# Kernel tuning notes

Hardware: AMD Instinct MI355X
Metric: run time of the kernel (lower is better)

Reference implementation:

```python
import jax, jax.numpy as jnp
import numpy as np
from jax import lax

DIM = 192
HEADS = 4
HIDDEN = int(DIM * 2.66)  # 510
B, H, W = 2, 64, 64
EPS_LN = 1e-6
EPS_NORM = 1e-12


def conv1x1(x, w, b):
    # x: (b,c,h,w), w: (o,c), b: (o,)
    return jnp.einsum('bchw,oc->bohw', x, w) + b[None, :, None, None]


def dwconv3x3(x, w, b):
    # depthwise 3x3, SAME padding; w: (C,1,3,3)
    c = x.shape[1]
    y = lax.conv_general_dilated(x, w, window_strides=(1, 1), padding='SAME',
                                 feature_group_count=c,
                                 dimension_numbers=('NCHW', 'OIHW', 'NCHW'))
    return y + b[None, :, None, None]


def layernorm2d(x, w, b):
    mean = jnp.mean(x, axis=(2, 3), keepdims=True)
    var = jnp.mean((x - mean) ** 2, axis=(2, 3), keepdims=True)
    return (x - mean) / jnp.sqrt(var + EPS_LN) * w[None, :, None, None] + b[None, :, None, None]


def mdta(x, qkv_w, qkv_b, qkv_dw_w, qkv_dw_b, temperature, proj_w, proj_b):
    b, c, h, w = x.shape
    qkv = dwconv3x3(conv1x1(x, qkv_w, qkv_b), qkv_dw_w, qkv_dw_b)
    q, k, v = jnp.split(qkv, 3, axis=1)
    dh = c // HEADS
    q = q.reshape(b, HEADS, dh, h * w)
    k = k.reshape(b, HEADS, dh, h * w)
    v = v.reshape(b, HEADS, dh, h * w)
    # L2-normalize over per-head channel dim (axis=2), like F.normalize(dim=2)
    q = q / jnp.maximum(jnp.linalg.norm(q, axis=2, keepdims=True), EPS_NORM)
    k = k / jnp.maximum(jnp.linalg.norm(k, axis=2, keepdims=True), EPS_NORM)
    # spatial attention map: (b, heads, HW, HW)
    attn = jnp.einsum('bhcn,bhcm->bhnm', q, k) * temperature[None]  # temp (heads,1,1)
    attn = jax.nn.softmax(attn, axis=-1)
    out = jnp.einsum('bhnm,bhcm->bhcn', attn, v)  # (b,heads,dh,HW)
    out = out.reshape(b, c, h, w)
    return conv1x1(out, proj_w, proj_b)


def gdfn(x, pin_w, pin_b, dw_w, dw_b, pout_w, pout_b):
    y = dwconv3x3(conv1x1(x, pin_w, pin_b), dw_w, dw_b)
    y1, y2 = jnp.split(y, 2, axis=1)
    y = jax.nn.gelu(y1, approximate=False) * y2
    return conv1x1(y, pout_w, pout_b)


def setup_inputs() -> dict:
    key = jax.random.key(0)
    ks = jax.random.split(key, 8)
    s = 0.02
    return {
        'x': jax.random.normal(ks[0], (B, DIM, H, W), jnp.float32),
        'ln1_w': jnp.ones((DIM,), jnp.float32),
        'ln1_b': jnp.zeros((DIM,), jnp.float32),
        'qkv_w': jax.random.normal(ks[1], (DIM * 3, DIM), jnp.float32) * s,
        'qkv_b': jnp.zeros((DIM * 3,), jnp.float32),
        'qkv_dw_w': jax.random.normal(ks[2], (DIM * 3, 1, 3, 3), jnp.float32) * s,
        'qkv_dw_b': jnp.zeros((DIM * 3,), jnp.float32),
        'temperature': jnp.ones((HEADS, 1, 1), jnp.float32),
        'proj_w': jax.random.normal(ks[3], (DIM, DIM), jnp.float32) * s,
        'proj_b': jnp.zeros((DIM,), jnp.float32),
        'ln2_w': jnp.ones((DIM,), jnp.float32),
        'ln2_b': jnp.zeros((DIM,), jnp.float32),
        'pin_w': jax.random.normal(ks[4], (HIDDEN * 2, DIM), jnp.float32) * s,
        'pin_b': jnp.zeros((HIDDEN * 2,), jnp.float32),
        'gdfn_dw_w': jax.random.normal(ks[5], (HIDDEN * 2, 1, 3, 3), jnp.float32) * s,
        'gdfn_dw_b': jnp.zeros((HIDDEN * 2,), jnp.float32),
        'pout_w': jax.random.normal(ks[6], (DIM, HIDDEN), jnp.float32) * s,
        'pout_b': jnp.zeros((DIM,), jnp.float32),
    }


def reference(x, ln1_w, ln1_b, qkv_w, qkv_b, qkv_dw_w, qkv_dw_b, temperature,
              proj_w, proj_b, ln2_w, ln2_b, pin_w, pin_b, gdfn_dw_w, gdfn_dw_b,
              pout_w, pout_b):
    x = x + mdta(layernorm2d(x, ln1_w, ln1_b), qkv_w, qkv_b, qkv_dw_w, qkv_dw_b,
                 temperature, proj_w, proj_b)
    x = x + gdfn(layernorm2d(x, ln2_w, ln2_b), pin_w, pin_b, gdfn_dw_w, gdfn_dw_b,
                 pout_w, pout_b)
    return x
```

## Files before the change

### kernel.cpp

```cpp
#include <hip/hip_runtime.h>
#include <hip/hip_bf16.h>

typedef __bf16 bf16x8 __attribute__((ext_vector_type(8)));
typedef __bf16 bf16x4 __attribute__((ext_vector_type(4)));
typedef __bf16 bf16x2 __attribute__((ext_vector_type(2)));
typedef float f32x4 __attribute__((ext_vector_type(4)));

#define HW 4096
#define DIMC 192
#define DH 48
#define HIDC 510
#define LOG2E 1.44269504088896f

__device__ __forceinline__ float exp2_fast(float x) {
#if __has_builtin(__builtin_amdgcn_exp2f)
  return __builtin_amdgcn_exp2f(x);
#else
  float r;
  asm("v_exp_f32 %0, %1\n\ts_nop 1" : "=v"(r) : "v"(x));
  return r;
#endif
}

__device__ __forceinline__ float rcp_fast(float x) {
#if __has_builtin(__builtin_amdgcn_rcpf)
  return __builtin_amdgcn_rcpf(x);
#else
  float r;
  asm("v_rcp_f32 %0, %1\n\ts_nop 1" : "=v"(r) : "v"(x));
  return r;
#endif
}

__device__ __forceinline__ float gelu_fast(float x) {
  float z = fabsf(x) * 0.70710678118654752f;
  float t = rcp_fast(fmaf(0.3275911f, z, 1.f));
  float p = t * fmaf(t, fmaf(t, fmaf(t, fmaf(t, 1.061405429f, -1.453152027f), 1.421413741f), -0.284496736f), 0.254829592f);
  float e = exp2_fast(-z * z * 1.4426950408889634f);
  float erfa = 1.f - p * e;
  float erfx = copysignf(erfa, x);
  return 0.5f * x * (1.f + erfx);
}

__global__ __launch_bounds__(256) void wcvt_ln_kernel(const float* __restrict__ qkv_w, const float* __restrict__ proj_w,
                                                      const float* __restrict__ pin_w, const float* __restrict__ pout_w,
                                                      __bf16* __restrict__ wb_qkv, __bf16* __restrict__ wb_proj,
                                                      __bf16* __restrict__ wb_pin, __bf16* __restrict__ wb_pout,
                                                      const float* __restrict__ x, const float* __restrict__ lw,
                                                      const float* __restrict__ lb, float* __restrict__ sc,
                                                      float* __restrict__ sh) {
  __shared__ float red[8];
  if (blockIdx.x < 1725) {
    int idx = blockIdx.x * 256 + threadIdx.x;
    if (idx < 110592) {
      wb_qkv[idx] = (__bf16)qkv_w[idx];
    } else if (idx < 147456) {
      int i = idx - 110592;
      wb_proj[i] = (__bf16)proj_w[i];
    } else if (idx < 343296) {
      int i = idx - 147456;
      wb_pin[i] = (__bf16)pin_w[i];
    } else if (idx < 441600) {
      int i = idx - 343296;
      int o = i >> 9, c = i & 511;
      wb_pout[i] = (c < HIDC) ? (__bf16)pout_w[o * HIDC + c] : (__bf16)0.f;
    }
    return;
  }
  int bc = blockIdx.x - 1725;
  int c = bc % DIMC;
  const float* row = x + (size_t)bc * HW;
  float s = 0.f, s2 = 0.f;
  for (int i = threadIdx.x * 4; i < HW; i += 1024) {
    f32x4 v = *(const f32x4*)&row[i];
    s += (v.x + v.y) + (v.z + v.w);
    s2 = fmaf(v.x, v.x, s2); s2 = fmaf(v.y, v.y, s2);
    s2 = fmaf(v.z, v.z, s2); s2 = fmaf(v.w, v.w, s2);
  }
  for (int off = 32; off; off >>= 1) { s += __shfl_down(s, off, 64); s2 += __shfl_down(s2, off, 64); }
  int wid = threadIdx.x >> 6;
  if ((threadIdx.x & 63) == 0) { red[wid] = s; red[4 + wid] = s2; }
  __syncthreads();
  if (threadIdx.x == 0) {
    s = red[0] + red[1] + red[2] + red[3];
    s2 = red[4] + red[5] + red[6] + red[7];
    float mean = s * (1.f / HW);
    float var = s2 * (1.f / HW) - mean * mean;
    float rstd = rsqrtf(var + 1e-6f);
    float scv = rstd * lw[c];
    sc[bc] = scv;
    sh[bc] = lb[c] - mean * scv;
  }
}

__global__ __launch_bounds__(256) void ln_stats_kernel(const float* __restrict__ x, const float* __restrict__ w,
                                                       const float* __restrict__ b, float* __restrict__ sc,
                                                       float* __restrict__ sh) {
  int bc = blockIdx.x;
  int c = bc % DIMC;
  const float* row = x + (size_t)bc * HW;
  float s = 0.f, s2 = 0.f;
  for (int i = threadIdx.x * 4; i < HW; i += 1024) {
    f32x4 v = *(const f32x4*)&row[i];
    s += (v.x + v.y) + (v.z + v.w);
    s2 = fmaf(v.x, v.x, s2); s2 = fmaf(v.y, v.y, s2);
    s2 = fmaf(v.z, v.z, s2); s2 = fmaf(v.w, v.w, s2);
  }
  __shared__ float red[8];
  for (int off = 32; off; off >>= 1) { s += __shfl_down(s, off, 64); s2 += __shfl_down(s2, off, 64); }
  int wid = threadIdx.x >> 6;
  if ((threadIdx.x & 63) == 0) { red[wid] = s; red[4 + wid] = s2; }
  __syncthreads();
  if (threadIdx.x == 0) {
    s = red[0] + red[1] + red[2] + red[3];
    s2 = red[4] + red[5] + red[6] + red[7];
    float mean = s * (1.f / HW);
    float var = s2 * (1.f / HW) - mean * mean;
    float rstd = rsqrtf(var + 1e-6f);
    float scv = rstd * w[c];
    sc[bc] = scv;
    sh[bc] = b[c] - mean * scv;
  }
}

__global__ __launch_bounds__(256) void ln_apply_t_kernel(const float* __restrict__ x, const float* __restrict__ sc,
                                                         const float* __restrict__ sh, __bf16* __restrict__ Xt) {
  int n0 = blockIdx.x * 64, c0 = blockIdx.y * 32, b = blockIdx.z;
  int t = threadIdx.x;
  int n = t & 63, cs = c0 + (t >> 6) * 8;
  __bf16 ob[8];
#pragma unroll
  for (int cc = 0; cc < 8; ++cc) {
    int c = cs + cc;
    float v = fmaf(x[((size_t)(b * DIMC + c)) * HW + n0 + n], sc[b * DIMC + c], sh[b * DIMC + c]);
    ob[cc] = (__bf16)v;
  }
  *(bf16x8*)&Xt[((size_t)((b << 12) + n0 + n)) * DIMC + cs] = *(bf16x8*)ob;
}

__global__ __launch_bounds__(256) void gemm_kernel(const __bf16* __restrict__ A, const __bf16* __restrict__ Bt,
                                                   const float* __restrict__ bias, const float* __restrict__ res,
                                                   float* __restrict__ outf, __bf16* __restrict__ outb,
                                                   const float* __restrict__ part,
                                                   int O, int Cs, int mode) {
  __shared__ __align__(16) __bf16 Asub[64 * 72];
  __shared__ __align__(16) __bf16 Bsub[128 * 72];
  __shared__ float linvS[4][128];
  const int t = threadIdx.x;
  const int lane = t & 63, wv = t >> 6;
  const int q4 = lane >> 4, l16 = lane & 15;
  int o0 = blockIdx.y * 64;
  if (o0 + 64 > O) o0 = O - 64;
  const int ntot0 = blockIdx.x * 128;
  const int b = ntot0 >> 12;
  const int n_in_b0 = ntot0 & 4095;

  if (mode == 4) {
#pragma unroll
    for (int jj = 0; jj < 2; ++jj) {
      int id = t + 256 * jj;
      int h = id >> 7, nl = id & 127;
      int n_in_b = n_in_b0 + nl;
      int ntb = n_in_b >> 6, n64 = n_in_b & 63;
      size_t pb = ((size_t)((b * 4 + h) * 64 + ntb)) * 3136 + 3072 + n64;
      float s = part[pb] + part[pb + (size_t)512 * 3136];
      linvS[h][nl] = rcp_fast(s);
    }
  }

  f32x4 acc[8];
#pragma unroll
  for (int nt = 0; nt < 8; ++nt) acc[nt] = (f32x4){0.f, 0.f, 0.f, 0.f};

  for (int c0 = 0; c0 < Cs; c0 += 64) {
    __syncthreads();
#pragma unroll
    for (int j = 0; j < 2; ++j) {
      int id = t + 256 * j;
      *(bf16x8*)&Asub[(id >> 3) * 72 + (id & 7) * 8] =
          *(const bf16x8*)&A[((size_t)(o0 + (id >> 3))) * Cs + c0 + (id & 7) * 8];
    }
    if (mode == 4) {
#pragma unroll
      for (int j = 0; j < 4; ++j) {
        int id = t + 256 * j;
        int row = id >> 3, cgrp = id & 7;
        int cglob = c0 + cgrp * 8;
        int h = cglob / 48;
        int cc = cglob - h * 48;
        int n_in_b = n_in_b0 + row;
        int ntb = n_in_b >> 6, n64 = n_in_b & 63;
        size_t pb = ((size_t)((b * 4 + h) * 64 + ntb)) * 3136 + (size_t)n64 * 48 + cc;
        f32x4 a0 = *(const f32x4*)&part[pb];
        f32x4 a1 = *(const f32x4*)&part[pb + 4];
        f32x4 b0 = *(const f32x4*)&part[pb + (size_t)512 * 3136];
        f32x4 b1 = *(const f32x4*)&part[pb + (size_t)512 * 3136 + 4];
        float li = linvS[h][row];
        f32x4 s0 = (a0 + b0) * li;
        f32x4 s1 = (a1 + b1) * li;
        bf16x8 ov = { (__bf16)s0.x, (__bf16)s0.y, (__bf16)s0.z, (__bf16)s0.w,
                      (__bf16)s1.x, (__bf16)s1.y, (__bf16)s1.z, (__bf16)s1.w };
        *(bf16x8*)&Bsub[row * 72 + cgrp * 8] = ov;
      }
    } else if (mode != 3) {
#pragma unroll
      for (int j = 0; j < 4; ++j) {
        int id = t + 256 * j;
        *(bf16x8*)&Bsub[(id >> 3) * 72 + (id & 7) * 8] =
            *(const bf16x8*)&Bt[((size_t)(ntot0 + (id >> 3))) * Cs + c0 + (id & 7) * 8];
      }
    } else {
      int cr = t & 63, seg = t >> 6;
      int cg = c0 + cr;
      __bf16 tmp[32];
      if (cg < HIDC) {
        const __bf16* gp = Bt + ((size_t)(b * HIDC + cg)) * HW + n_in_b0 + seg * 32;
#pragma unroll
        for (int j = 0; j < 4; ++j) *(bf16x8*)&tmp[8 * j] = *(const bf16x8*)&gp[8 * j];
      } else {
#pragma unroll
        for (int k = 0; k < 32; ++k) tmp[k] = (__bf16)0.f;
      }
#pragma unroll
      for (int k = 0; k < 32; ++k) Bsub[(seg * 32 + k) * 72 + cr] = tmp[k];
    }
    __syncthreads();
#pragma unroll
    for (int ks = 0; ks < 2; ++ks) {
      bf16x8 af = *(const bf16x8*)&Asub[(16 * wv + l16) * 72 + 32 * ks + 8 * q4];
#pragma unroll
      for (int nt = 0; nt < 8; ++nt) {
        bf16x8 bfr = *(const bf16x8*)&Bsub[(16 * nt + l16) * 72 + 32 * ks + 8 * q4];
        acc[nt] = __builtin_amdgcn_mfma_f32_16x16x32_bf16(af, bfr, acc[nt], 0, 0, 0);
      }
    }
  }

  float bvals[4];
#pragma unroll
  for (int r = 0; r < 4; ++r) bvals[r] = bias[o0 + 16 * wv + 4 * q4 + r];
#pragma unroll
  for (int nt = 0; nt < 8; ++nt) {
    int n_in_b = n_in_b0 + 16 * nt + l16;
#pragma unroll
    for (int r = 0; r < 4; ++r) {
      int o = o0 + 16 * wv + 4 * q4 + r;
      size_t addr = ((size_t)(b * O + o)) * HW + n_in_b;
      float v = acc[nt][r] + bvals[r];
      if (mode >= 2) { outf[addr] = v + res[addr]; }
      else if (mode == 0) { outf[addr] = v; }
      else { outb[addr] = (__bf16)v; }
    }
  }
}

__global__ __launch_bounds__(256) void dwconv_split_kernel(const __bf16* __restrict__ in, const float* __restrict__ w,
                                                           const float* __restrict__ bias,
                                                           __bf16* __restrict__ qdwb, __bf16* __restrict__ Vbf) {
  int bc = blockIdx.x;
  int b = bc / 576, ch = bc - b * 576;
  __shared__ float tile[66 * 68];
  for (int i = threadIdx.x; i < 66 * 68; i += 256) tile[i] = 0.f;
  __syncthreads();
  const __bf16* p = in + (size_t)bc * HW;
  for (int j = 0; j < 8; ++j) {
    int i = 2 * threadIdx.x + 512 * j;
    bf16x2 v = *(const bf16x2*)&p[i];
    int y = i >> 6, xx = i & 63;
    tile[(y + 1) * 68 + xx + 1] = (float)v.x;
    tile[(y + 1) * 68 + xx + 2] = (float)v.y;
  }
  __syncthreads();
  float w0 = w[ch * 9 + 0], w1 = w[ch * 9 + 1], w2 = w[ch * 9 + 2];
  float w3 = w[ch * 9 + 3], w4 = w[ch * 9 + 4], w5 = w[ch * 9 + 5];
  float w6 = w[ch * 9 + 6], w7 = w[ch * 9 + 7], w8 = w[ch * 9 + 8];
  float bb = bias[ch];
  __bf16* dst;
  if (ch < 384) dst = qdwb + ((size_t)(b * 384 + ch)) * HW;
  else {
    int c = ch - 384, h = c / DH, cc = c - h * DH;
    dst = Vbf + ((size_t)((b * 4 + h) * DH + cc)) * HW;
  }
  for (int j = 0; j < 8; ++j) {
    int i = 2 * threadIdx.x + 512 * j;
    int y = i >> 6, xx = i & 63;
    const float* tt = &tile[y * 68 + xx];
    float a = bb;
    a = fmaf(w0, tt[0], a);   a = fmaf(w1, tt[1], a);   a = fmaf(w2, tt[2], a);
    a = fmaf(w3, tt[68], a);  a = fmaf(w4, tt[69], a);  a = fmaf(w5, tt[70], a);
    a = fmaf(w6, tt[136], a); a = fmaf(w7, tt[137], a); a = fmaf(w8, tt[138], a);
    float a2 = bb;
    a2 = fmaf(w0, tt[1], a2);   a2 = fmaf(w1, tt[2], a2);   a2 = fmaf(w2, tt[3], a2);
    a2 = fmaf(w3, tt[69], a2);  a2 = fmaf(w4, tt[70], a2);  a2 = fmaf(w5, tt[71], a2);
    a2 = fmaf(w6, tt[137], a2); a2 = fmaf(w7, tt[138], a2); a2 = fmaf(w8, tt[139], a2);
    bf16x2 o = { (__bf16)a, (__bf16)a2 };
    *(bf16x2*)&dst[i] = o;
  }
}

__global__ __launch_bounds__(256) void gdfn_dw_gate_kernel(const __bf16* __restrict__ hid, const float* __restrict__ w,
                                                           const float* __restrict__ bias, __bf16* __restrict__ gate) {
  int blk = blockIdx.x;
  int b = blk / HIDC, j = blk - b * HIDC;
  __shared__ __align__(16) float t1[66 * 68];
  __shared__ __align__(16) float t2[66 * 68];
  const int tid = threadIdx.x;
  if (tid < 136) {
    int r = (tid >= 68) ? 65 : 0;
    int c = (tid >= 68) ? tid - 68 : tid;
    t1[r * 68 + c] = 0.f;
    t2[r * 68 + c] = 0.f;
  }
  {
    int r = (tid >> 2) + 1;
    int c4 = tid & 3;
    int c = (c4 == 0) ? 0 : 64 + c4;
    t1[r * 68 + c] = 0.f;
    t2[r * 68 + c] = 0.f;
  }
  const __bf16* p1 = hid + ((size_t)b * (2 * HIDC) + j) * HW;
  const __bf16* p2 = p1 + (size_t)HIDC * HW;
  for (int jj = 0; jj < 8; ++jj) {
    int i = 2 * tid + 512 * jj;
    bf16x2 v1 = *(const bf16x2*)&p1[i];
    bf16x2 v2 = *(const bf16x2*)&p2[i];
    int y = i >> 6, xx = i & 63;
    t1[(y + 1) * 68 + xx + 1] = (float)v1.x;
    t1[(y + 1) * 68 + xx + 2] = (float)v1.y;
    t2[(y + 1) * 68 + xx + 1] = (float)v2.x;
    t2[(y + 1) * 68 + xx + 2] = (float)v2.y;
  }
  __syncthreads();
  int c1 = j, c2 = j + HIDC;
  float wa[9], wb[9];
#pragma unroll
  for (int k = 0; k < 9; ++k) { wa[k] = w[c1 * 9 + k]; wb[k] = w[c2 * 9 + k]; }
  float bi1 = bias[c1], bi2 = bias[c2];

  const int y = tid >> 2, x0 = 16 * (tid & 3);
  float x1v[16], x2v[16];
#pragma unroll
  for (int p = 0; p < 16; ++p) { x1v[p] = bi1; x2v[p] = bi2; }
#pragma unroll
  for (int r = 0; r < 3; ++r) {
    const float* rp1 = &t1[(y + r) * 68 + x0];
    float rr[20];
#pragma unroll
    for (int q = 0; q < 5; ++q) *(f32x4*)&rr[4 * q] = *(const f32x4*)&rp1[4 * q];
    float w0 = wa[3 * r], w1 = wa[3 * r + 1], w2 = wa[3 * r + 2];
#pragma unroll
    for (int p = 0; p < 16; ++p)
      x1v[p] = fmaf(w0, rr[p], fmaf(w1, rr[p + 1], fmaf(w2, rr[p + 2], x1v[p])));
  }
#pragma unroll
  for (int r = 0; r < 3; ++r) {
    const float* rp2 = &t2[(y + r) * 68 + x0];
    float rr[20];
#pragma unroll
    for (int q = 0; q < 5; ++q) *(f32x4*)&rr[4 * q] = *(const f32x4*)&rp2[4 * q];
    float w0 = wb[3 * r], w1 = wb[3 * r + 1], w2 = wb[3 * r + 2];
#pragma unroll
    for (int p = 0; p < 16; ++p)
      x2v[p] = fmaf(w0, rr[p], fmaf(w1, rr[p + 1], fmaf(w2, rr[p + 2], x2v[p])));
  }
  __bf16 ob[16];
#pragma unroll
  for (int p = 0; p < 16; ++p) ob[p] = (__bf16)(gelu_fast(x1v[p]) * x2v[p]);
  __bf16* op = gate + ((size_t)b * HIDC + j) * HW + y * 64 + x0;
  *(bf16x8*)&op[0] = *(bf16x8*)&ob[0];
  *(bf16x8*)&op[8] = *(bf16x8*)&ob[8];
}

__global__ __launch_bounds__(256) void prep_qk_kernel(const __bf16* __restrict__ qdwb, const float* __restrict__ temp,
                                                      __bf16* __restrict__ Qbf, __bf16* __restrict__ Kbf) {
  int t2 = blockIdx.x * 256 + threadIdx.x;
  int bh = t2 >> 11;
  int np = (t2 & 2047) * 2;
  int b = bh >> 2, h = bh & 3;
  const int isK = blockIdx.y;
  const __bf16* sp = qdwb + ((size_t)(b * 384 + isK * 192 + h * DH)) * HW + np;
  float tq = isK ? 1.f : temp[h] * LOG2E;

  bf16x2 raw[DH];
  float ss0 = 0.f, ss1 = 0.f;
#pragma unroll
  for (int c = 0; c < DH; ++c) {
    bf16x2 v = *(const bf16x2*)&sp[(size_t)c * HW];
    raw[c] = v;
    float f0 = (float)v.x, f1 = (float)v.y;
    ss0 = fmaf(f0, f0, ss0);
    ss1 = fmaf(f1, f1, ss1);
  }
  float sc0 = tq / fmaxf(sqrtf(ss0), 1e-12f);
  float sc1 = tq / fmaxf(sqrtf(ss1), 1e-12f);
  __bf16 ob0[64], ob1[64];
#pragma unroll
  for (int c = 0; c < DH; ++c) {
    ob0[c] = (__bf16)((float)raw[c].x * sc0);
    ob1[c] = (__bf16)((float)raw[c].y * sc1);
  }
#pragma unroll
  for (int c = DH; c < 64; ++c) { ob0[c] = (__bf16)0.f; ob1[c] = (__bf16)0.f; }
  __bf16* dd = (isK ? Kbf : Qbf) + ((size_t)(bh << 12) + np) * 64;
#pragma unroll
  for (int ch = 0; ch < 8; ++ch) {
    *(bf16x8*)&dd[ch * 8] = *(bf16x8*)&ob0[ch * 8];
    *(bf16x8*)&dd[64 + ch * 8] = *(bf16x8*)&ob1[ch * 8];
  }
}

__global__ __launch_bounds__(256) void attn_split_kernel(const __bf16* __restrict__ Qbf, const __bf16* __restrict__ Kbf,
                                                         const __bf16* __restrict__ Vbf, float* __restrict__ part) {
  __shared__ __align__(16) __bf16 Vc[2][48 * 72];
  __shared__ __align__(16) __bf16 Pl[2][64 * 72];
  const int tid = threadIdx.x;
  const int lane = tid & 63;
  const int wv = tid >> 6;
  const int q4 = lane >> 4, l16 = lane & 15;
  const int bid = blockIdx.x;
  const int chunk = bid >> 9, rest = bid & 511;
  const int bh = rest >> 6, nt = rest & 63;
  const int n0 = nt * 64;
  const __bf16* Qg = Qbf + (size_t)bh * HW * 64;
  const __bf16* Kg = Kbf + (size_t)bh * HW * 64;
  const __bf16* Vg = Vbf + (size_t)bh * DH * HW;

  bf16x8 qf[4][2];
#pragma unroll
  for (int s = 0; s < 4; ++s)
#pragma unroll
    for (int ks = 0; ks < 2; ++ks)
      qf[s][ks] = *(const bf16x8*)&Qg[((size_t)(n0 + 16 * s + l16)) * 64 + 32 * ks + 8 * q4];

  const int m0 = chunk * 2048;
  const __bf16* kp0 = Kg + ((size_t)(m0 + 16 * wv + l16)) * 64 + 8 * q4;
  const __bf16* kp1 = kp0 + 32;
  const __bf16* vp0 = Vg + ((size_t)(tid >> 3)) * HW + m0 + (tid & 7) * 8;
  const __bf16* vp1 = Vg + ((size_t)((tid + 256) >> 3)) * HW + m0 + ((tid + 256) & 7) * 8;
  bf16x8 kf0 = *(const bf16x8*)kp0;
  bf16x8 kf1 = *(const bf16x8*)kp1;
  bf16x8 vreg[2];
  vreg[0] = *(const bf16x8*)vp0;
  if (tid < 128) vreg[1] = *(const bf16x8*)vp1;

  float lsub[4] = {0.f, 0.f, 0.f, 0.f};
  f32x4 oacc[3];
#pragma unroll
  for (int ct = 0; ct < 3; ++ct) oacc[ct] = (f32x4){0.f, 0.f, 0.f, 0.f};

  for (int it = 0; it < 32; ++it) {
    const int cur = it & 1;
    *(bf16x8*)&Vc[cur][(tid >> 3) * 72 + (tid & 7) * 8] = vreg[0];
    if (tid < 128) {
      int i = tid + 256;
      *(bf16x8*)&Vc[cur][(i >> 3) * 72 + (i & 7) * 8] = vreg[1];
    }
    kp0 += 4096; kp1 += 4096; vp0 += 64; vp1 += 64;
    bf16x8 kn0 = *(const bf16x8*)kp0;
    bf16x8 kn1 = *(const bf16x8*)kp1;
    vreg[0] = *(const bf16x8*)vp0;
    if (tid < 128) vreg[1] = *(const bf16x8*)vp1;

    f32x4 sacc[4];
#pragma unroll
    for (int s = 0; s < 4; ++s) sacc[s] = (f32x4){0.f, 0.f, 0.f, 0.f};
    __builtin_amdgcn_s_setprio(1);
#pragma unroll
    for (int s = 0; s < 4; ++s)
      sacc[s] = __builtin_amdgcn_mfma_f32_16x16x32_bf16(kf0, qf[s][0], sacc[s], 0, 0, 0);
#pragma unroll
    for (int s = 0; s < 4; ++s)
      sacc[s] = __builtin_amdgcn_mfma_f32_16x16x32_bf16(kf1, qf[s][1], sacc[s], 0, 0, 0);
    __builtin_amdgcn_s_setprio(0);

#pragma unroll
    for (int s = 0; s < 4; ++s) {
      float p0 = exp2_fast(sacc[s][0]);
      float p1 = exp2_fast(sacc[s][1]);
      float p2 = exp2_fast(sacc[s][2]);
      float p3 = exp2_fast(sacc[s][3]);
      lsub[s] += (p0 + p1) + (p2 + p3);
      bf16x4 pk = { (__bf16)p0, (__bf16)p1, (__bf16)p2, (__bf16)p3 };
      *(bf16x4*)&Pl[cur][(16 * s + l16) * 72 + 16 * wv + 4 * q4] = pk;
    }
    __syncthreads();

    __builtin_amdgcn_s_setprio(1);
#pragma unroll
    for (int ks = 0; ks < 2; ++ks) {
      bf16x8 pf = *(const bf16x8*)&Pl[cur][(16 * wv + l16) * 72 + 32 * ks + 8 * q4];
#pragma unroll
      for (int ct = 0; ct < 3; ++ct) {
        bf16x8 vf = *(const bf16x8*)&Vc[cur][(16 * ct + l16) * 72 + 32 * ks + 8 * q4];
        oacc[ct] = __builtin_amdgcn_mfma_f32_16x16x32_bf16(pf, vf, oacc[ct], 0, 0, 0);
      }
    }
    __builtin_amdgcn_s_setprio(0);
    kf0 = kn0; kf1 = kn1;
  }

  __syncthreads();
  float* Lred = (float*)&Pl[0][0];
#pragma unroll
  for (int s = 0; s < 4; ++s) {
    float v = lsub[s];
    v += __shfl_xor(v, 16, 64);
    v += __shfl_xor(v, 32, 64);
    if (q4 == 0) Lred[wv * 64 + 16 * s + l16] = v;
  }
  __syncthreads();
  size_t pbase = (size_t)bid * 3136;
  if (tid < 64)
    part[pbase + 3072 + tid] = Lred[tid] + Lred[64 + tid] + Lred[128 + tid] + Lred[192 + tid];
#pragma unroll
  for (int ct = 0; ct < 3; ++ct)
#pragma unroll
    for (int r = 0; r < 4; ++r) {
      int n = 16 * wv + 4 * q4 + r;
      part[pbase + (size_t)n * 48 + 16 * ct + l16] = oacc[ct][r];
    }
}

extern "C" void kernel_launch(void* const* d_in, const int* in_sizes, int n_in,
                              void* d_out, int out_size, void* d_ws, size_t ws_size,
                              hipStream_t stream) {
  const float* x        = (const float*)d_in[0];
  const float* ln1_w    = (const float*)d_in[1];
  const float* ln1_b    = (const float*)d_in[2];
  const float* qkv_w    = (const float*)d_in[3];
  const float* qkv_b    = (const float*)d_in[4];
  const float* qkv_dw_w = (const float*)d_in[5];
  const float* qkv_dw_b = (const float*)d_in[6];
  const float* temperature = (const float*)d_in[7];
  const float* proj_w   = (const float*)d_in[8];
  const float* proj_b   = (const float*)d_in[9];
  const float* ln2_w    = (const float*)d_in[10];
  const float* ln2_b    = (const float*)d_in[11];
  const float* pin_w    = (const float*)d_in[12];
  const float* pin_b    = (const float*)d_in[13];
  const float* gdfn_dw_w = (const float*)d_in[14];
  const float* gdfn_dw_b = (const float*)d_in[15];
  const float* pout_w   = (const float*)d_in[16];
  const float* pout_b   = (const float*)d_in[17];
  float* out = (float*)d_out;
  float* ws = (float*)d_ws;

  __bf16* wb_qkv  = (__bf16*)(ws + 0);
  __bf16* wb_proj = (__bf16*)(ws + 55296);
  __bf16* wb_pin  = (__bf16*)(ws + 73728);
  __bf16* wb_pout = (__bf16*)(ws + 171648);
  float* sc1 = ws + 220800;
  float* sh1 = ws + 221184;
  float* sc2 = ws + 221568;
  float* sh2 = ws + 221952;
  __bf16* Xt1 = (__bf16*)(ws + 222336);
  __bf16* Xt2 = (__bf16*)(ws + 222336);
  __bf16* Qbf = (__bf16*)(ws + 222336);
  __bf16* Kbf = (__bf16*)(ws + 1270912);
  __bf16* Vbf = (__bf16*)(ws + 2319488);
  __bf16* qkvb   = (__bf16*)(ws + 3105920);
  __bf16* hid    = (__bf16*)(ws + 3105920);
  __bf16* qdwb  = (__bf16*)(ws + 5465216);
  float*  Opart = ws + 5465216;
  __bf16* gate  = (__bf16*)(ws + 7283840);

  wcvt_ln_kernel<<<1725 + 2 * DIMC, 256, 0, stream>>>(qkv_w, proj_w, pin_w, pout_w,
                                                      wb_qkv, wb_proj, wb_pin, wb_pout,
                                                      x, ln1_w, ln1_b, sc1, sh1);
  ln_apply_t_kernel<<<dim3(64, 6, 2), 256, 0, stream>>>(x, sc1, sh1, Xt1);
  gemm_kernel<<<dim3(64, 9), 256, 0, stream>>>(wb_qkv, Xt1, qkv_b, nullptr, nullptr, qkvb, nullptr, 576, 192, 1);
  dwconv_split_kernel<<<1152, 256, 0, stream>>>(qkvb, qkv_dw_w, qkv_dw_b, qdwb, Vbf);
  prep_qk_kernel<<<dim3(64, 2), 256, 0, stream>>>(qdwb, temperature, Qbf, Kbf);
  attn_split_kernel<<<1024, 256, 0, stream>>>(Qbf, Kbf, Vbf, Opart);
  gemm_kernel<<<dim3(64, 3), 256, 0, stream>>>(wb_proj, nullptr, proj_b, x, out, nullptr, Opart, 192, 192, 4);

  ln_stats_kernel<<<2 * DIMC, 256, 0, stream>>>(out, ln2_w, ln2_b, sc2, sh2);
  ln_apply_t_kernel<<<dim3(64, 6, 2), 256, 0, stream>>>(out, sc2, sh2, Xt2);
  gemm_kernel<<<dim3(64, 16), 256, 0, stream>>>(wb_pin, Xt2, pin_b, nullptr, nullptr, hid, nullptr, 1020, 192, 1);
  gdfn_dw_gate_kernel<<<2 * HIDC, 256, 0, stream>>>(hid, gdfn_dw_w, gdfn_dw_b, gate);
  gemm_kernel<<<dim3(64, 3), 256, 0, stream>>>(wb_pout, (const __bf16*)gate, pout_b, out, out, nullptr, nullptr, 192, 512, 3);
}
```

Before: 238.2 us.

## Fuse layernorm apply into GEMM B-tile load and widen prep_qk grid

```diff
diff --git a/kernel.cpp b/kernel.cpp
--- a/kernel.cpp
+++ b/kernel.cpp
@@ -123,25 +123,11 @@
   }
 }
 
-__global__ __launch_bounds__(256) void ln_apply_t_kernel(const float* __restrict__ x, const float* __restrict__ sc,
-                                                         const float* __restrict__ sh, __bf16* __restrict__ Xt) {
-  int n0 = blockIdx.x * 64, c0 = blockIdx.y * 32, b = blockIdx.z;
-  int t = threadIdx.x;
-  int n = t & 63, cs = c0 + (t >> 6) * 8;
-  __bf16 ob[8];
-#pragma unroll
-  for (int cc = 0; cc < 8; ++cc) {
-    int c = cs + cc;
-    float v = fmaf(x[((size_t)(b * DIMC + c)) * HW + n0 + n], sc[b * DIMC + c], sh[b * DIMC + c]);
-    ob[cc] = (__bf16)v;
-  }
-  *(bf16x8*)&Xt[((size_t)((b << 12) + n0 + n)) * DIMC + cs] = *(bf16x8*)ob;
-}
-
 __global__ __launch_bounds__(256) void gemm_kernel(const __bf16* __restrict__ A, const __bf16* __restrict__ Bt,
                                                    const float* __restrict__ bias, const float* __restrict__ res,
                                                    float* __restrict__ outf, __bf16* __restrict__ outb,
                                                    const float* __restrict__ part,
+                                                   const float* __restrict__ scp, const float* __restrict__ shp,
                                                    int O, int Cs, int mode) {
   __shared__ __align__(16) __bf16 Asub[64 * 72];
   __shared__ __align__(16) __bf16 Bsub[128 * 72];
@@ -202,6 +188,16 @@
                       (__bf16)s1.x, (__bf16)s1.y, (__bf16)s1.z, (__bf16)s1.w };
         *(bf16x8*)&Bsub[row * 72 + cgrp * 8] = ov;
       }
+    } else if (mode == 5) {
+      int cr = t & 63, seg = t >> 6;
+      int cglob = c0 + cr;
+      const float* xp = part + ((size_t)(b * DIMC + cglob)) * HW + n_in_b0 + seg * 32;
+      float scv = scp[b * DIMC + cglob], shv = shp[b * DIMC + cglob];
+      float rr[32];
+#pragma unroll
+      for (int q = 0; q < 8; ++q) *(f32x4*)&rr[4 * q] = *(const f32x4*)&xp[4 * q];
+#pragma unroll
+      for (int k = 0; k < 32; ++k) Bsub[(seg * 32 + k) * 72 + cr] = (__bf16)fmaf(rr[k], scv, shv);
     } else if (mode != 3) {
 #pragma unroll
       for (int j = 0; j < 4; ++j) {
@@ -247,7 +243,7 @@
       int o = o0 + 16 * wv + 4 * q4 + r;
       size_t addr = ((size_t)(b * O + o)) * HW + n_in_b;
       float v = acc[nt][r] + bvals[r];
-      if (mode >= 2) { outf[addr] = v + res[addr]; }
+      if (mode >= 2 && mode <= 4) { outf[addr] = v + res[addr]; }
       else if (mode == 0) { outf[addr] = v; }
       else { outb[addr] = (__bf16)v; }
     }
@@ -374,39 +370,31 @@
 __global__ __launch_bounds__(256) void prep_qk_kernel(const __bf16* __restrict__ qdwb, const float* __restrict__ temp,
                                                       __bf16* __restrict__ Qbf, __bf16* __restrict__ Kbf) {
   int t2 = blockIdx.x * 256 + threadIdx.x;
-  int bh = t2 >> 11;
-  int np = (t2 & 2047) * 2;
+  int bh = t2 >> 12;
+  int np = t2 & 4095;
   int b = bh >> 2, h = bh & 3;
   const int isK = blockIdx.y;
   const __bf16* sp = qdwb + ((size_t)(b * 384 + isK * 192 + h * DH)) * HW + np;
   float tq = isK ? 1.f : temp[h] * LOG2E;
 
-  bf16x2 raw[DH];
-  float ss0 = 0.f, ss1 = 0.f;
+  __bf16 raw[DH];
+  float ss = 0.f;
 #pragma unroll
   for (int c = 0; c < DH; ++c) {
-    bf16x2 v = *(const bf16x2*)&sp[(size_t)c * HW];
+    __bf16 v = sp[(size_t)c * HW];
     raw[c] = v;
-    float f0 = (float)v.x, f1 = (float)v.y;
-    ss0 = fmaf(f0, f0, ss0);
-    ss1 = fmaf(f1, f1, ss1);
-  }
-  float sc0 = tq / fmaxf(sqrtf(ss0), 1e-12f);
-  float sc1 = tq / fmaxf(sqrtf(ss1), 1e-12f);
-  __bf16 ob0[64], ob1[64];
-#pragma unroll
-  for (int c = 0; c < DH; ++c) {
-    ob0[c] = (__bf16)((float)raw[c].x * sc0);
-    ob1[c] = (__bf16)((float)raw[c].y * sc1);
-  }
-#pragma unroll
-  for (int c = DH; c < 64; ++c) { ob0[c] = (__bf16)0.f; ob1[c] = (__bf16)0.f; }
+    float f = (float)v;
+    ss = fmaf(f, f, ss);
+  }
+  float scv = tq / fmaxf(sqrtf(ss), 1e-12f);
+  __bf16 ob[64];
+#pragma unroll
+  for (int c = 0; c < DH; ++c) ob[c] = (__bf16)((float)raw[c] * scv);
+#pragma unroll
+  for (int c = DH; c < 64; ++c) ob[c] = (__bf16)0.f;
   __bf16* dd = (isK ? Kbf : Qbf) + ((size_t)(bh << 12) + np) * 64;
 #pragma unroll
-  for (int ch = 0; ch < 8; ++ch) {
-    *(bf16x8*)&dd[ch * 8] = *(bf16x8*)&ob0[ch * 8];
-    *(bf16x8*)&dd[64 + ch * 8] = *(bf16x8*)&ob1[ch * 8];
-  }
+  for (int ch = 0; ch < 8; ++ch) *(bf16x8*)&dd[ch * 8] = *(bf16x8*)&ob[ch * 8];
 }
 
 __global__ __launch_bounds__(256) void attn_split_kernel(const __bf16* __restrict__ Qbf, const __bf16* __restrict__ Kbf,
@@ -553,8 +541,6 @@
   float* sh1 = ws + 221184;
   float* sc2 = ws + 221568;
   float* sh2 = ws + 221952;
-  __bf16* Xt1 = (__bf16*)(ws + 222336);
-  __bf16* Xt2 = (__bf16*)(ws + 222336);
   __bf16* Qbf = (__bf16*)(ws + 222336);
   __bf16* Kbf = (__bf16*)(ws + 1270912);
   __bf16* Vbf = (__bf16*)(ws + 2319488);
@@ -567,16 +553,18 @@
   wcvt_ln_kernel<<<1725 + 2 * DIMC, 256, 0, stream>>>(qkv_w, proj_w, pin_w, pout_w,
                                                       wb_qkv, wb_proj, wb_pin, wb_pout,
                                                       x, ln1_w, ln1_b, sc1, sh1);
-  ln_apply_t_kernel<<<dim3(64, 6, 2), 256, 0, stream>>>(x, sc1, sh1, Xt1);
-  gemm_kernel<<<dim3(64, 9), 256, 0, stream>>>(wb_qkv, Xt1, qkv_b, nullptr, nullptr, qkvb, nullptr, 576, 192, 1);
+  gemm_kernel<<<dim3(64, 9), 256, 0, stream>>>(wb_qkv, nullptr, qkv_b, nullptr, nullptr, qkvb,
+                                               x, sc1, sh1, 576, 192, 5);
   dwconv_split_kernel<<<1152, 256, 0, stream>>>(qkvb, qkv_dw_w, qkv_dw_b, qdwb, Vbf);
-  prep_qk_kernel<<<dim3(64, 2), 256, 0, stream>>>(qdwb, temperature, Qbf, Kbf);
+  prep_qk_kernel<<<dim3(128, 2), 256, 0, stream>>>(qdwb, temperature, Qbf, Kbf);
   attn_split_kernel<<<1024, 256, 0, stream>>>(Qbf, Kbf, Vbf, Opart);
-  gemm_kernel<<<dim3(64, 3), 256, 0, stream>>>(wb_proj, nullptr, proj_b, x, out, nullptr, Opart, 192, 192, 4);
+  gemm_kernel<<<dim3(64, 3), 256, 0, stream>>>(wb_proj, nullptr, proj_b, x, out, nullptr,
+                                               Opart, nullptr, nullptr, 192, 192, 4);
 
   ln_stats_kernel<<<2 * DIMC, 256, 0, stream>>>(out, ln2_w, ln2_b, sc2, sh2);
-  ln_apply_t_kernel<<<dim3(64, 6, 2), 256, 0, stream>>>(out, sc2, sh2, Xt2);
-  gemm_kernel<<<dim3(64, 16), 256, 0, stream>>>(wb_pin, Xt2, pin_b, nullptr, nullptr, hid, nullptr, 1020, 192, 1);
+  gemm_kernel<<<dim3(64, 16), 256, 0, stream>>>(wb_pin, nullptr, pin_b, nullptr, nullptr, hid,
+                                                out, sc2, sh2, 1020, 192, 5);
   gdfn_dw_gate_kernel<<<2 * HIDC, 256, 0, stream>>>(hid, gdfn_dw_w, gdfn_dw_b, gate);
-  gemm_kernel<<<dim3(64, 3), 256, 0, stream>>>(wb_pout, (const __bf16*)gate, pout_b, out, out, nullptr, nullptr, 192, 512, 3);
-}
+  gemm_kernel<<<dim3(64, 3), 256, 0, stream>>>(wb_pout, (const __bf16*)gate, pout_b, out, out, nullptr,
+                                               nullptr, nullptr, nullptr, 192, 512, 3);
+}
```

Measured after the change: 256.4 us. 1.08x slower.
